# Kernel tuning notes

Measured on AMD Instinct MI355X. Metric: run time of the kernel, lower is better.

The kernel has to match this reference:

```python
import jax, jax.numpy as jnp
import numpy as np

N_NODES = 50000
NUM_FEATURES = 128
HIDDEN = 128
OUT = 64
N_EDGES = 600000


def gcn_conv(x, edge_index, W, b, n_nodes):
    """PyG GCNConv: add self-loops, symmetric deg^{-1/2} normalization,
    x' = D^{-1/2}(A+I)D^{-1/2} (x @ W) + b."""
    xw = x @ W  # [N, out]
    loop = jnp.arange(n_nodes, dtype=edge_index.dtype)
    row = jnp.concatenate([edge_index[0], loop])  # source
    col = jnp.concatenate([edge_index[1], loop])  # target
    ones = jnp.ones(row.shape[0], dtype=xw.dtype)
    deg = jax.ops.segment_sum(ones, col, num_segments=n_nodes)  # in-degree incl. self-loop
    dis = jnp.where(deg > 0, jax.lax.rsqrt(deg), 0.0)
    norm = dis[row] * dis[col]  # [E+N]
    msg = xw[row] * norm[:, None]  # gather + scale
    agg = jax.ops.segment_sum(msg, col, num_segments=n_nodes)  # scatter-add
    return agg + b


def setup_inputs() -> dict:
    key = jax.random.key(0)
    ks = jax.random.split(key, 10)
    x = jax.random.normal(ks[0], (N_NODES, NUM_FEATURES), dtype=jnp.float32)
    edge_index = jax.random.randint(ks[1], (2, N_EDGES), 0, N_NODES, dtype=jnp.int64)
    s1 = 1.0 / np.sqrt(NUM_FEATURES)
    s2 = 1.0 / np.sqrt(HIDDEN)
    s3 = 1.0 / np.sqrt(OUT)
    # encoder GCN weights stored as [in, out]
    W_enc1 = jax.random.uniform(ks[2], (NUM_FEATURES, HIDDEN), jnp.float32, -s1, s1)
    b_enc1 = jnp.zeros((HIDDEN,), jnp.float32)
    W_enc2 = jax.random.uniform(ks[3], (HIDDEN, OUT), jnp.float32, -s2, s2)
    b_enc2 = jnp.zeros((OUT,), jnp.float32)
    # decoder Linear weights stored as [in, out]
    W_dec1 = jax.random.uniform(ks[4], (OUT, HIDDEN), jnp.float32, -s3, s3)
    b_dec1 = jax.random.uniform(ks[5], (HIDDEN,), jnp.float32, -s3, s3)
    W_dec2 = jax.random.uniform(ks[6], (HIDDEN, NUM_FEATURES), jnp.float32, -s2, s2)
    b_dec2 = jax.random.uniform(ks[7], (NUM_FEATURES,), jnp.float32, -s2, s2)
    return {"x": x, "edge_index": edge_index,
            "W_enc1": W_enc1, "b_enc1": b_enc1,
            "W_enc2": W_enc2, "b_enc2": b_enc2,
            "W_dec1": W_dec1, "b_dec1": b_dec1,
            "W_dec2": W_dec2, "b_dec2": b_dec2}


def reference(x, edge_index, W_enc1, b_enc1, W_enc2, b_enc2,
              W_dec1, b_dec1, W_dec2, b_dec2):
    n = x.shape[0]
    z = jax.nn.relu(gcn_conv(x, edge_index, W_enc1, b_enc1, n))
    z = jax.nn.relu(gcn_conv(z, edge_index, W_enc2, b_enc2, n))
    z = jax.nn.relu(z @ W_dec1 + b_dec1)
    x_hat = z @ W_dec2 + b_dec2
    return x_hat
```

## Files before the change

kernel.cpp:

```cpp
#include <hip/hip_runtime.h>
#include <hip/hip_bf16.h>


#define N_FEAT 128
#define HID    128
#define OUTD   64

typedef __hip_bfloat16 bf16;
typedef unsigned short u16;
typedef __attribute__((ext_vector_type(8))) short short8;
typedef __attribute__((ext_vector_type(4))) float f32x4;

__device__ __forceinline__ float bs2f(short s) {
    return __builtin_bit_cast(float, ((unsigned)(unsigned short)s) << 16);
}
__device__ __forceinline__ short f2bs(float f) {
    __hip_bfloat16 h = __float2bfloat16(f);
    return __builtin_bit_cast(short, h);
}


__global__ void k_prep(int* __restrict__ cnt, int n, int ZB,
                       const float* __restrict__ W1, const float* __restrict__ W2,
                       const float* __restrict__ Wd1, const float* __restrict__ Wd2,
                       bf16* __restrict__ W1t, bf16* __restrict__ W2t,
                       bf16* __restrict__ Wd1t, bf16* __restrict__ Wd2t) {
    int b = blockIdx.x;
    if (b < ZB) {
        int i4 = b * 256 + threadIdx.x;
        int n4 = n >> 2;
        if (i4 < n4) ((int4*)cnt)[i4] = make_int4(0, 0, 0, 0);
        if (i4 == 0) for (int i = n4 * 4; i < n; ++i) cnt[i] = 0;
        return;
    }
    int i = (b - ZB) * 256 + threadIdx.x;
    if (i < 16384) {
        int k = i >> 7, nn = i & 127;
        W1t[nn * 128 + k] = __float2bfloat16(W1[i]);
    } else if (i < 24576) {
        int j = i - 16384; int k = j >> 6, nn = j & 63;
        W2t[nn * 128 + k] = __float2bfloat16(W2[j]);
    } else if (i < 32768) {
        int j = i - 24576; int k = j >> 7, nn = j & 127;
        Wd1t[nn * 64 + k] = __float2bfloat16(Wd1[j]);
    } else if (i < 49152) {
        int j = i - 32768; int k = j >> 7, nn = j & 127;
        Wd2t[nn * 128 + k] = __float2bfloat16(Wd2[j]);
    }
}


__global__ void k_mega(const int* __restrict__ row, const int* __restrict__ col,
                       int E, int SL, int npg, int GB,
                       int* __restrict__ cnt, u16* __restrict__ slots, int n,
                       const float* __restrict__ x, const bf16* __restrict__ W1t,
                       bf16* __restrict__ xw1) {
    int b = blockIdx.x;
    if (b < GB) {
        if (b * 64 >= n) return;
        int t = threadIdx.x;
        int lane = t & 63, w = t >> 6;
        int quad = lane >> 4, l16 = lane & 15;
        int m0 = b * 64 + (w & 1) * 32;
        int nhw = (w >> 1) * 32;
        int kq = quad * 8;

        short8 zero8 = {0, 0, 0, 0, 0, 0, 0, 0};
        int mrow[2]; bool mok[2];
#pragma unroll
        for (int mi = 0; mi < 2; ++mi) {
            mrow[mi] = m0 + mi * 16 + l16;
            mok[mi] = mrow[mi] < n;
        }
        short8 af[2][4];
#pragma unroll
        for (int mi = 0; mi < 2; ++mi) {
#pragma unroll
            for (int kb = 0; kb < 4; ++kb) {
                if (!mok[mi]) { af[mi][kb] = zero8; continue; }
                const float* Af = x + (size_t)mrow[mi] * 128 + kb * 32 + kq;
                float4 a4 = *(const float4*)Af;
                float4 b4 = *(const float4*)(Af + 4);
                short8 r = {f2bs(a4.x), f2bs(a4.y), f2bs(a4.z), f2bs(a4.w),
                            f2bs(b4.x), f2bs(b4.y), f2bs(b4.z), f2bs(b4.w)};
                af[mi][kb] = r;
            }
        }
#pragma unroll
        for (int nc = 0; nc < 128; nc += 64) {
            int n0 = nc + nhw;
            f32x4 acc[2][2];
#pragma unroll
            for (int mi = 0; mi < 2; ++mi)
#pragma unroll
                for (int ni = 0; ni < 2; ++ni)
#pragma unroll
                    for (int r = 0; r < 4; ++r) acc[mi][ni][r] = 0.f;
#pragma unroll
            for (int kb = 0; kb < 4; ++kb) {
                short8 bfm[2];
#pragma unroll
                for (int ni = 0; ni < 2; ++ni) {
                    int nn = n0 + ni * 16 + l16;
                    bfm[ni] = *(const short8*)(W1t + (size_t)nn * 128 + kb * 32 + kq);
                }
#pragma unroll
                for (int mi = 0; mi < 2; ++mi)
#pragma unroll
                    for (int ni = 0; ni < 2; ++ni)
                        acc[mi][ni] = __builtin_amdgcn_mfma_f32_16x16x32_bf16(
                            af[mi][kb], bfm[ni], acc[mi][ni], 0, 0, 0);
            }
#pragma unroll
            for (int ni = 0; ni < 2; ++ni) {
                int nn = n0 + ni * 16 + l16;
#pragma unroll
                for (int mi = 0; mi < 2; ++mi)
#pragma unroll
                    for (int r = 0; r < 4; ++r) {
                        int m = m0 + mi * 16 + quad * 4 + r;
                        if (m < n)
                            ((short*)xw1)[(size_t)m * 128 + nn] = f2bs(acc[mi][ni][r]);
                    }
            }
        }
        return;
    }
    int bb = b - GB;
    int g = bb & 7;
    int s = bb >> 3;
    int lo = g * npg;
    int hi = lo + npg; if (hi > n) hi = n;
    int i4 = s * 256 + threadIdx.x;
    int E4 = E >> 2;
    if (i4 < E4) {
        int4 r4 = ((const int4*)row)[i4];
        int4 c4 = ((const int4*)col)[i4];
        int rr[4] = {r4.x, r4.y, r4.z, r4.w};
        int cc[4] = {c4.x, c4.y, c4.z, c4.w};
#pragma unroll
        for (int u = 0; u < 4; ++u) {
            int r = rr[u], c = cc[u];
            if (c >= lo && c < hi && (unsigned)r < (unsigned)n) {
                int pos = atomicAdd(&cnt[c], 1);
                if (pos < 64) slots[(size_t)c * 64 + pos] = (u16)r;
            }
        }
    }
    if (i4 == 0) {
        for (int e = E4 * 4; e < E; ++e) {
            int r = row[e], c = col[e];
            if (c >= lo && c < hi && (unsigned)r < (unsigned)n) {
                int pos = atomicAdd(&cnt[c], 1);
                if (pos < 64) slots[(size_t)c * 64 + pos] = (u16)r;
            }
        }
    }
}


__global__ void k_aggmm(const bf16* __restrict__ xw1, const int* __restrict__ cnt,
                        const u16* __restrict__ slots, const float* __restrict__ b1,
                        const bf16* __restrict__ W2t, bf16* __restrict__ xw2, int M) {
    __shared__ short h1s[64][136];
    __shared__ u16 sl_s[64][72];
    __shared__ float dn_s[64];
    __shared__ int cn_s[64];
    int t = threadIdx.x;
    int lane = t & 63, w = t >> 6;
    int blk = blockIdx.x;

    if (t < 64) {
        int nd = blk * 64 + t;
        int craw = (nd < M) ? cnt[nd] : -1;
        cn_s[t] = (nd < M) ? (min(craw, 64) + 1) : 0;
        dn_s[t] = (nd < M) ? rsqrtf((float)(craw + 1)) : 0.f;
    }
    {
        int node = t >> 3, chunk = t & 7;
        int nd = blk * 64 + node;
        int4 val = make_int4(0, 0, 0, 0);
        if (nd < M)
            val = ((const int4*)(slots + (size_t)nd * 64))[chunk];
        *(int4*)&sl_s[node][chunk * 8] = val;
    }
    __syncthreads();

    int sub = lane >> 4, li = lane & 15;
    float4 c0 = *(const float4*)(b1 + li * 8);
    float4 c1 = *(const float4*)(b1 + li * 8 + 4);
    float bbv[8] = {c0.x, c0.y, c0.z, c0.w, c1.x, c1.y, c1.z, c1.w};

#pragma unroll
    for (int rnd = 0; rnd < 2; ++rnd) {
        int nl = w * 8 + rnd * 4 + sub;
        int nd = blk * 64 + nl;
        int cn = cn_s[nl];
        float a[8] = {0.f, 0.f, 0.f, 0.f, 0.f, 0.f, 0.f, 0.f};
        for (int tt = 0; tt < cn; tt += 8) {
            bool va[8]; short8 v[8]; float dsv[8];
#pragma unroll
            for (int u = 0; u < 8; ++u) {
                int ti = tt + u;
                va[u] = ti < cn;
                int tc = va[u] ? ti : 0;
                int sI = (tc == cn - 1) ? nd : (int)sl_s[nl][tc];
                v[u] = *((const short8*)(xw1 + (size_t)sI * 128) + li);
                dsv[u] = rsqrtf((float)(cnt[sI] + 1));
            }
#pragma unroll
            for (int u = 0; u < 8; ++u)
                if (va[u]) {
#pragma unroll
                    for (int j = 0; j < 8; ++j) a[j] += dsv[u] * bs2f(v[u][j]);
                }
        }
        float dn = dn_s[nl];
        short8 o;
#pragma unroll
        for (int j = 0; j < 8; ++j) o[j] = f2bs(fmaxf(dn * a[j] + bbv[j], 0.f));
        *(short8*)&h1s[nl][li * 8] = o;
    }
    __syncthreads();

    int quad = lane >> 4, l16 = lane & 15;
    int mt = w & 3;
    int nh = w >> 2;
    int kq = quad * 8;

    short8 af[4];
#pragma unroll
    for (int kb = 0; kb < 4; ++kb)
        af[kb] = *(const short8*)&h1s[mt * 16 + l16][kb * 32 + kq];

    f32x4 acc[2];
#pragma unroll
    for (int ni = 0; ni < 2; ++ni)
#pragma unroll
        for (int r = 0; r < 4; ++r) acc[ni][r] = 0.f;
#pragma unroll
    for (int kb = 0; kb < 4; ++kb) {
        short8 bfm[2];
#pragma unroll
        for (int ni = 0; ni < 2; ++ni) {
            int nn = nh * 32 + ni * 16 + l16;
            bfm[ni] = *(const short8*)(W2t + (size_t)nn * 128 + kb * 32 + kq);
        }
#pragma unroll
        for (int ni = 0; ni < 2; ++ni)
            acc[ni] = __builtin_amdgcn_mfma_f32_16x16x32_bf16(
                af[kb], bfm[ni], acc[ni], 0, 0, 0);
    }
#pragma unroll
    for (int ni = 0; ni < 2; ++ni) {
        int nn = nh * 32 + ni * 16 + l16;
#pragma unroll
        for (int r = 0; r < 4; ++r) {
            int ml = mt * 16 + quad * 4 + r;
            int m = blk * 64 + ml;
            if (m < M)
                ((short*)xw2)[(size_t)m * 64 + nn] = f2bs(acc[ni][r] * dn_s[ml]);
        }
    }
}


__global__ void k_aggdec(const bf16* __restrict__ xw2, const int* __restrict__ cnt,
                         const u16* __restrict__ slots,
                         const float* __restrict__ b2,
                         const bf16* __restrict__ Wd1t, const float* __restrict__ bd1,
                         const bf16* __restrict__ Wd2t, const float* __restrict__ bd2,
                         float* __restrict__ out, int M) {
    __shared__ short h2s[64][72];
    __shared__ short h3s[64][136];
    __shared__ u16 sl_s[64][72];
    __shared__ float dn_s[64];
    __shared__ int cn_s[64];
    int t = threadIdx.x;
    int lane = t & 63, w = t >> 6;
    int blk = blockIdx.x;

    if (t < 64) {
        int nd = blk * 64 + t;
        int craw = (nd < M) ? cnt[nd] : -1;
        cn_s[t] = (nd < M) ? (min(craw, 64) + 1) : 0;
        dn_s[t] = (nd < M) ? rsqrtf((float)(craw + 1)) : 0.f;
    }
    {
        int node = t >> 3, chunk = t & 7;
        int nd = blk * 64 + node;
        int4 val = make_int4(0, 0, 0, 0);
        if (nd < M)
            val = ((const int4*)(slots + (size_t)nd * 64))[chunk];
        *(int4*)&sl_s[node][chunk * 8] = val;
    }
    __syncthreads();

    {
        int grp = t >> 3, li = t & 7;
        int nd = blk * 64 + grp;
        int cn = cn_s[grp];
        float a[8] = {0.f, 0.f, 0.f, 0.f, 0.f, 0.f, 0.f, 0.f};
        for (int tt = 0; tt < cn; tt += 8) {
            bool va[8]; short8 v[8];
#pragma unroll
            for (int u = 0; u < 8; ++u) {
                int ti = tt + u;
                va[u] = ti < cn;
                int tc = va[u] ? ti : 0;
                int sI = (tc == cn - 1) ? nd : (int)sl_s[grp][tc];
                v[u] = *((const short8*)(xw2 + (size_t)sI * 64) + li);
            }
#pragma unroll
            for (int u = 0; u < 8; ++u)
                if (va[u]) {
#pragma unroll
                    for (int j = 0; j < 8; ++j) a[j] += bs2f(v[u][j]);
                }
        }
        float dn = dn_s[grp];
        float4 c0 = *(const float4*)(b2 + li * 8);
        float4 c1 = *(const float4*)(b2 + li * 8 + 4);
        float bb[8] = {c0.x, c0.y, c0.z, c0.w, c1.x, c1.y, c1.z, c1.w};
        short8 o;
#pragma unroll
        for (int j = 0; j < 8; ++j) o[j] = f2bs(fmaxf(dn * a[j] + bb[j], 0.f));
        *(short8*)&h2s[grp][li * 8] = o;
    }
    __syncthreads();

    int quad = lane >> 4, l16 = lane & 15;
    int mt = w & 3;
    int nh = w >> 2;
    int kq = quad * 8;

    {
        short8 af1[2];
#pragma unroll
        for (int kb = 0; kb < 2; ++kb)
            af1[kb] = *(const short8*)&h2s[mt * 16 + l16][kb * 32 + kq];

        f32x4 acc[4];
#pragma unroll
        for (int ni = 0; ni < 4; ++ni)
#pragma unroll
            for (int r = 0; r < 4; ++r) acc[ni][r] = 0.f;
#pragma unroll
        for (int kb = 0; kb < 2; ++kb) {
            short8 bfm[4];
#pragma unroll
            for (int ni = 0; ni < 4; ++ni) {
                int nn = nh * 64 + ni * 16 + l16;
                bfm[ni] = *(const short8*)(Wd1t + (size_t)nn * OUTD + kb * 32 + kq);
            }
#pragma unroll
            for (int ni = 0; ni < 4; ++ni)
                acc[ni] = __builtin_amdgcn_mfma_f32_16x16x32_bf16(
                    af1[kb], bfm[ni], acc[ni], 0, 0, 0);
        }
#pragma unroll
        for (int ni = 0; ni < 4; ++ni) {
            int nn = nh * 64 + ni * 16 + l16;
            float bv = bd1[nn];
#pragma unroll
            for (int r = 0; r < 4; ++r) {
                int ml = mt * 16 + quad * 4 + r;
                h3s[ml][nn] = f2bs(fmaxf(acc[ni][r] + bv, 0.f));
            }
        }
    }
    __syncthreads();

    {
        short8 af2[4];
#pragma unroll
        for (int kb = 0; kb < 4; ++kb)
            af2[kb] = *(const short8*)&h3s[mt * 16 + l16][kb * 32 + kq];

        f32x4 acc[4];
#pragma unroll
        for (int ni = 0; ni < 4; ++ni)
#pragma unroll
            for (int r = 0; r < 4; ++r) acc[ni][r] = 0.f;
#pragma unroll
        for (int kb = 0; kb < 4; ++kb) {
            short8 bfm[4];
#pragma unroll
            for (int ni = 0; ni < 4; ++ni) {
                int nn = nh * 64 + ni * 16 + l16;
                bfm[ni] = *(const short8*)(Wd2t + (size_t)nn * HID + kb * 32 + kq);
            }
#pragma unroll
            for (int ni = 0; ni < 4; ++ni)
                acc[ni] = __builtin_amdgcn_mfma_f32_16x16x32_bf16(
                    af2[kb], bfm[ni], acc[ni], 0, 0, 0);
        }
#pragma unroll
        for (int ni = 0; ni < 4; ++ni) {
            int nn = nh * 64 + ni * 16 + l16;
            float bv = bd2[nn];
#pragma unroll
            for (int r = 0; r < 4; ++r) {
                int m = blk * 64 + mt * 16 + quad * 4 + r;
                if (m < M)
                    out[(size_t)m * N_FEAT + nn] = acc[ni][r] + bv;
            }
        }
    }
}


extern "C" void kernel_launch(void* const* d_in, const int* in_sizes, int n_in,
                              void* d_out, int out_size, void* d_ws, size_t ws_size,
                              hipStream_t stream) {
    const float* x   = (const float*)d_in[0];
    const int*   ei  = (const int*)d_in[1];
    const float* W1  = (const float*)d_in[2];
    const float* b1  = (const float*)d_in[3];
    const float* W2  = (const float*)d_in[4];
    const float* b2  = (const float*)d_in[5];
    const float* Wd1 = (const float*)d_in[6];
    const float* bd1 = (const float*)d_in[7];
    const float* Wd2 = (const float*)d_in[8];
    const float* bd2 = (const float*)d_in[9];

    const int n = in_sizes[0] / N_FEAT;
    const int E = in_sizes[1] / 2;
    const int* row = ei;
    const int* col = ei + E;

    char* wp = (char*)d_ws;
    bf16* xw1 = (bf16*)wp;  wp += (size_t)n * 128 * 2;
    bf16* xw2 = (bf16*)wp;  wp += (size_t)n * 64 * 2;
    bf16* W1t = (bf16*)wp;  wp += 128 * 128 * 2;
    bf16* W2t = (bf16*)wp;  wp += 128 * 64 * 2;
    bf16* Wd1t= (bf16*)wp;  wp += 64 * 128 * 2;
    bf16* Wd2t= (bf16*)wp;  wp += 128 * 128 * 2;
    int* cnt   = (int*)wp;   wp += (size_t)n * 4;
    u16* slots = (u16*)wp;   wp += (size_t)n * 64 * 2;

    int ZB = (n + 1023) / 1024;
    k_prep<<<ZB + 192, 256, 0, stream>>>(cnt, n, ZB, W1, W2, Wd1, Wd2,
                                         W1t, W2t, Wd1t, Wd2t);

    int E4 = E >> 2;
    int SL = (E4 + 255) / 256;
    int npg = (n + 7) / 8;
    int mg = (n + 63) / 64;
    int GB = (mg + 7) & ~7;
    k_mega<<<GB + 8 * SL, 256, 0, stream>>>(row, col, E, SL, npg, GB,
                                            cnt, slots, n, x, W1t, xw1);

    k_aggmm<<<mg, 512, 0, stream>>>(xw1, cnt, slots, b1, W2t, xw2, n);

    k_aggdec<<<mg, 512, 0, stream>>>(xw2, cnt, slots, b2,
                                     Wd1t, bd1, Wd2t, bd2, (float*)d_out, n);
}
```

Baseline: 193.0 us.

## Aggregate raw bf16 features before first GEMM, fusing W1 matmul into aggregation kernel

After: 205.5 us. +6.5%, slower.

```diff
diff --git a/kernel.cpp b/kernel.cpp
--- a/kernel.cpp
+++ b/kernel.cpp
@@ -50,79 +50,20 @@
 }
 
 
-__global__ void k_mega(const int* __restrict__ row, const int* __restrict__ col,
-                       int E, int SL, int npg, int GB,
-                       int* __restrict__ cnt, u16* __restrict__ slots, int n,
-                       const float* __restrict__ x, const bf16* __restrict__ W1t,
-                       bf16* __restrict__ xw1) {
+__global__ void k_edgecast(const int* __restrict__ row, const int* __restrict__ col,
+                           int E, int SL, int npg, int GB,
+                           int* __restrict__ cnt, u16* __restrict__ slots, int n,
+                           const float* __restrict__ x, bf16* __restrict__ xb) {
     int b = blockIdx.x;
     if (b < GB) {
-        if (b * 64 >= n) return;
-        int t = threadIdx.x;
-        int lane = t & 63, w = t >> 6;
-        int quad = lane >> 4, l16 = lane & 15;
-        int m0 = b * 64 + (w & 1) * 32;
-        int nhw = (w >> 1) * 32;
-        int kq = quad * 8;
-
-        short8 zero8 = {0, 0, 0, 0, 0, 0, 0, 0};
-        int mrow[2]; bool mok[2];
-#pragma unroll
-        for (int mi = 0; mi < 2; ++mi) {
-            mrow[mi] = m0 + mi * 16 + l16;
-            mok[mi] = mrow[mi] < n;
-        }
-        short8 af[2][4];
-#pragma unroll
-        for (int mi = 0; mi < 2; ++mi) {
-#pragma unroll
-            for (int kb = 0; kb < 4; ++kb) {
-                if (!mok[mi]) { af[mi][kb] = zero8; continue; }
-                const float* Af = x + (size_t)mrow[mi] * 128 + kb * 32 + kq;
-                float4 a4 = *(const float4*)Af;
-                float4 b4 = *(const float4*)(Af + 4);
-                short8 r = {f2bs(a4.x), f2bs(a4.y), f2bs(a4.z), f2bs(a4.w),
-                            f2bs(b4.x), f2bs(b4.y), f2bs(b4.z), f2bs(b4.w)};
-                af[mi][kb] = r;
-            }
-        }
-#pragma unroll
-        for (int nc = 0; nc < 128; nc += 64) {
-            int n0 = nc + nhw;
-            f32x4 acc[2][2];
-#pragma unroll
-            for (int mi = 0; mi < 2; ++mi)
-#pragma unroll
-                for (int ni = 0; ni < 2; ++ni)
-#pragma unroll
-                    for (int r = 0; r < 4; ++r) acc[mi][ni][r] = 0.f;
-#pragma unroll
-            for (int kb = 0; kb < 4; ++kb) {
-                short8 bfm[2];
-#pragma unroll
-                for (int ni = 0; ni < 2; ++ni) {
-                    int nn = n0 + ni * 16 + l16;
-                    bfm[ni] = *(const short8*)(W1t + (size_t)nn * 128 + kb * 32 + kq);
-                }
-#pragma unroll
-                for (int mi = 0; mi < 2; ++mi)
-#pragma unroll
-                    for (int ni = 0; ni < 2; ++ni)
-                        acc[mi][ni] = __builtin_amdgcn_mfma_f32_16x16x32_bf16(
-                            af[mi][kb], bfm[ni], acc[mi][ni], 0, 0, 0);
-            }
-#pragma unroll
-            for (int ni = 0; ni < 2; ++ni) {
-                int nn = n0 + ni * 16 + l16;
-#pragma unroll
-                for (int mi = 0; mi < 2; ++mi)
-#pragma unroll
-                    for (int r = 0; r < 4; ++r) {
-                        int m = m0 + mi * 16 + quad * 4 + r;
-                        if (m < n)
-                            ((short*)xw1)[(size_t)m * 128 + nn] = f2bs(acc[mi][ni][r]);
-                    }
-            }
+        int i = b * 2048 + threadIdx.x * 8;
+        int nF = n * N_FEAT;
+        if (i + 8 <= nF) {
+            float4 a4 = *(const float4*)(x + i);
+            float4 b4 = *(const float4*)(x + i + 4);
+            short8 r = {f2bs(a4.x), f2bs(a4.y), f2bs(a4.z), f2bs(a4.w),
+                        f2bs(b4.x), f2bs(b4.y), f2bs(b4.z), f2bs(b4.w)};
+            *(short8*)((short*)xb + i) = r;
         }
         return;
     }
@@ -159,9 +100,11 @@
 }
 
 
-__global__ void k_aggmm(const bf16* __restrict__ xw1, const int* __restrict__ cnt,
-                        const u16* __restrict__ slots, const float* __restrict__ b1,
-                        const bf16* __restrict__ W2t, bf16* __restrict__ xw2, int M) {
+__global__ void k_agg1(const bf16* __restrict__ xb, const int* __restrict__ cnt,
+                       const u16* __restrict__ slots, const float* __restrict__ b1,
+                       const bf16* __restrict__ W1t, const bf16* __restrict__ W2t,
+                       bf16* __restrict__ xw2, int M) {
+    __shared__ short aggXs[64][136];
     __shared__ short h1s[64][136];
     __shared__ u16 sl_s[64][72];
     __shared__ float dn_s[64];
@@ -187,10 +130,6 @@
     __syncthreads();
 
     int sub = lane >> 4, li = lane & 15;
-    float4 c0 = *(const float4*)(b1 + li * 8);
-    float4 c1 = *(const float4*)(b1 + li * 8 + 4);
-    float bbv[8] = {c0.x, c0.y, c0.z, c0.w, c1.x, c1.y, c1.z, c1.w};
-
 #pragma unroll
     for (int rnd = 0; rnd < 2; ++rnd) {
         int nl = w * 8 + rnd * 4 + sub;
@@ -205,7 +144,7 @@
                 va[u] = ti < cn;
                 int tc = va[u] ? ti : 0;
                 int sI = (tc == cn - 1) ? nd : (int)sl_s[nl][tc];
-                v[u] = *((const short8*)(xw1 + (size_t)sI * 128) + li);
+                v[u] = *((const short8*)(xb + (size_t)sI * 128) + li);
                 dsv[u] = rsqrtf((float)(cnt[sI] + 1));
             }
 #pragma unroll
@@ -218,8 +157,8 @@
         float dn = dn_s[nl];
         short8 o;
 #pragma unroll
-        for (int j = 0; j < 8; ++j) o[j] = f2bs(fmaxf(dn * a[j] + bbv[j], 0.f));
-        *(short8*)&h1s[nl][li * 8] = o;
+        for (int j = 0; j < 8; ++j) o[j] = f2bs(dn * a[j]);
+        *(short8*)&aggXs[nl][li * 8] = o;
     }
     __syncthreads();
 
@@ -228,38 +167,77 @@
     int nh = w >> 2;
     int kq = quad * 8;
 
-    short8 af[4];
-#pragma unroll
-    for (int kb = 0; kb < 4; ++kb)
-        af[kb] = *(const short8*)&h1s[mt * 16 + l16][kb * 32 + kq];
-
-    f32x4 acc[2];
-#pragma unroll
-    for (int ni = 0; ni < 2; ++ni)
-#pragma unroll
-        for (int r = 0; r < 4; ++r) acc[ni][r] = 0.f;
-#pragma unroll
-    for (int kb = 0; kb < 4; ++kb) {
-        short8 bfm[2];
+    {
+        short8 af[4];
+#pragma unroll
+        for (int kb = 0; kb < 4; ++kb)
+            af[kb] = *(const short8*)&aggXs[mt * 16 + l16][kb * 32 + kq];
+
+        f32x4 acc[4];
+#pragma unroll
+        for (int ni = 0; ni < 4; ++ni)
+#pragma unroll
+            for (int r = 0; r < 4; ++r) acc[ni][r] = 0.f;
+#pragma unroll
+        for (int kb = 0; kb < 4; ++kb) {
+            short8 bfm[4];
+#pragma unroll
+            for (int ni = 0; ni < 4; ++ni) {
+                int nn = nh * 64 + ni * 16 + l16;
+                bfm[ni] = *(const short8*)(W1t + (size_t)nn * 128 + kb * 32 + kq);
+            }
+#pragma unroll
+            for (int ni = 0; ni < 4; ++ni)
+                acc[ni] = __builtin_amdgcn_mfma_f32_16x16x32_bf16(
+                    af[kb], bfm[ni], acc[ni], 0, 0, 0);
+        }
+#pragma unroll
+        for (int ni = 0; ni < 4; ++ni) {
+            int nn = nh * 64 + ni * 16 + l16;
+            float bv = b1[nn];
+#pragma unroll
+            for (int r = 0; r < 4; ++r) {
+                int ml = mt * 16 + quad * 4 + r;
+                h1s[ml][nn] = f2bs(fmaxf(acc[ni][r] + bv, 0.f));
+            }
+        }
+    }
+    __syncthreads();
+
+    {
+        short8 af[4];
+#pragma unroll
+        for (int kb = 0; kb < 4; ++kb)
+            af[kb] = *(const short8*)&h1s[mt * 16 + l16][kb * 32 + kq];
+
+        f32x4 acc[2];
+#pragma unroll
+        for (int ni = 0; ni < 2; ++ni)
+#pragma unroll
+            for (int r = 0; r < 4; ++r) acc[ni][r] = 0.f;
+#pragma unroll
+        for (int kb = 0; kb < 4; ++kb) {
+            short8 bfm[2];
+#pragma unroll
+            for (int ni = 0; ni < 2; ++ni) {
+                int nn = nh * 32 + ni * 16 + l16;
+                bfm[ni] = *(const short8*)(W2t + (size_t)nn * 128 + kb * 32 + kq);
+            }
+#pragma unroll
+            for (int ni = 0; ni < 2; ++ni)
+                acc[ni] = __builtin_amdgcn_mfma_f32_16x16x32_bf16(
+                    af[kb], bfm[ni], acc[ni], 0, 0, 0);
+        }
 #pragma unroll
         for (int ni = 0; ni < 2; ++ni) {
             int nn = nh * 32 + ni * 16 + l16;
-            bfm[ni] = *(const short8*)(W2t + (size_t)nn * 128 + kb * 32 + kq);
-        }
-#pragma unroll
-        for (int ni = 0; ni < 2; ++ni)
-            acc[ni] = __builtin_amdgcn_mfma_f32_16x16x32_bf16(
-                af[kb], bfm[ni], acc[ni], 0, 0, 0);
-    }
-#pragma unroll
-    for (int ni = 0; ni < 2; ++ni) {
-        int nn = nh * 32 + ni * 16 + l16;
-#pragma unroll
-        for (int r = 0; r < 4; ++r) {
-            int ml = mt * 16 + quad * 4 + r;
-            int m = blk * 64 + ml;
-            if (m < M)
-                ((short*)xw2)[(size_t)m * 64 + nn] = f2bs(acc[ni][r] * dn_s[ml]);
+#pragma unroll
+            for (int r = 0; r < 4; ++r) {
+                int ml = mt * 16 + quad * 4 + r;
+                int m = blk * 64 + ml;
+                if (m < M)
+                    ((short*)xw2)[(size_t)m * 64 + nn] = f2bs(acc[ni][r] * dn_s[ml]);
+            }
         }
     }
 }
@@ -430,7 +408,7 @@
     const int* col = ei + E;
 
     char* wp = (char*)d_ws;
-    bf16* xw1 = (bf16*)wp;  wp += (size_t)n * 128 * 2;
+    bf16* xb  = (bf16*)wp;  wp += (size_t)n * 128 * 2;
     bf16* xw2 = (bf16*)wp;  wp += (size_t)n * 64 * 2;
     bf16* W1t = (bf16*)wp;  wp += 128 * 128 * 2;
     bf16* W2t = (bf16*)wp;  wp += 128 * 64 * 2;
@@ -446,12 +424,15 @@
     int E4 = E >> 2;
     int SL = (E4 + 255) / 256;
     int npg = (n + 7) / 8;
+    int nF = n * N_FEAT;
+    int CB = (nF + 2047) / 2048;
+    int GB = (CB + 7) & ~7;
+    k_edgecast<<<GB + 8 * SL, 256, 0, stream>>>(row, col, E, SL, npg, GB,
+                                                cnt, slots, n, x, xb);
+
     int mg = (n + 63) / 64;
-    int GB = (mg + 7) & ~7;
-    k_mega<<<GB + 8 * SL, 256, 0, stream>>>(row, col, E, SL, npg, GB,
-                                            cnt, slots, n, x, W1t, xw1);
-
-    k_aggmm<<<mg, 512, 0, stream>>>(xw1, cnt, slots, b1, W2t, xw2, n);
+
+    k_agg1<<<mg, 512, 0, stream>>>(xb, cnt, slots, b1, W1t, W2t, xw2, n);
 
     k_aggdec<<<mg, 512, 0, stream>>>(xw2, cnt, slots, b2,
                                      Wd1t, bd1, Wd2t, bd2, (float*)d_out, n);
```
